# Optimization experiments

Measured on AMD Instinct MI355X. Metric: run time of the kernel, lower is better.

The kernel has to match this reference:

```python
import jax, jax.numpy as jnp
import numpy as np

N_ENTITIES = 100000
N_RELATIONS = 1000
D = 100   # embedding_size
K = 4     # tensor slices
B = 4096  # batch


def setup_inputs() -> dict:
    key = jax.random.key(0)
    k1, k2, k3, k4, k5, k6, k7, k8 = jax.random.split(key, 8)
    return {
        "heads": jax.random.randint(k1, (B,), 0, N_ENTITIES),
        "tails": jax.random.randint(k2, (B,), 0, N_ENTITIES),
        "relations": jax.random.randint(k3, (B,), 0, N_RELATIONS),
        # parameters, matching tf.random_uniform(0, 1)
        "entity_embedding": jax.random.uniform(k4, (N_ENTITIES, D), dtype=jnp.float32),
        "W": jax.random.uniform(k5, (N_RELATIONS, K, D, D), dtype=jnp.float32),
        "V": jax.random.uniform(k6, (N_RELATIONS, K, 2 * D), dtype=jnp.float32),
        "Bp": jax.random.uniform(k7, (N_RELATIONS, K), dtype=jnpp_f32 if False else jnp.float32),
        "U": jax.random.uniform(k8, (N_RELATIONS, K), dtype=jnp.float32),
    }


def reference(heads, tails, relations, entity_embedding, W, V, Bp, U):
    # gathers
    e1 = entity_embedding[heads]          # [B, D]
    e2 = entity_embedding[tails]          # [B, D]
    w = W[relations]                      # [B, K, D, D]
    v = V[relations]                      # [B, K, 2D]
    b = Bp[relations]                     # [B, K]
    u = U[relations]                      # [B, K]

    # g_a = v @ [e1; e2]
    e12 = jnp.concatenate([e1, e2], axis=1)           # [B, 2D]
    g_a = jnp.einsum('bkm,bm->bk', v, e12)            # [B, K]
    # g_b = e1^T W_k e2 (bilinear tensor product)
    g_b = jnp.einsum('bd,bkde,be->bk', e1, w, e2)     # [B, K]

    score = jnp.einsum('bk,bk->b', u, jnp.tanh(g_a + g_b + b))  # [B]
    pred = jax.nn.sigmoid(score)
    return pred
```

## Files before the change

kernel.cpp:

```cpp
#include <hip/hip_runtime.h>
#include <math.h>

#define D 100
#define K 4
#define NREL 1000
#define CH 8
#define NT 512

__global__ __launch_bounds__(1024) void k_group(
    const int* __restrict__ rels, const int* __restrict__ heads,
    const int* __restrict__ tails, int B,
    int* __restrict__ start, int* __restrict__ bb,
    int* __restrict__ bh, int* __restrict__ bt)
{
    __shared__ int sA[1024], sB[1024];
    const int tid = threadIdx.x;
    sA[tid] = 0;
    __syncthreads();
    for (int b = tid; b < B; b += 1024) atomicAdd(&sA[rels[b]], 1);
    __syncthreads();
    const int v = sA[tid];
    int* src = sA; int* dst = sB;
    for (int off = 1; off < 1024; off <<= 1) {
        int x = src[tid];
        if (tid >= off) x += src[tid - off];
        dst[tid] = x;
        __syncthreads();
        int* t = src; src = dst; dst = t;
    }
    const int excl = src[tid] - v;
    if (tid < NREL) start[tid] = excl;
    if (tid == 0)   start[NREL] = B;
    int* cur = dst;
    cur[tid] = excl;
    __syncthreads();
    for (int b = tid; b < B; b += 1024) {
        const int r = rels[b];
        const int pos = atomicAdd(&cur[r], 1);
        bb[pos] = b;
        bh[pos] = heads[b];
        bt[pos] = tails[b];
    }
}

#define WLOAD(u) const float4 wv##u = Wg4[(bat10 + (u)*2 + dsub) * 25 + c];
#define WFMA(u) { \
    const int drow = gbase + bat10 + (u)*2 + dsub; \
    _Pragma("unroll") \
    for (int it = 0; it < CH; ++it) { \
        acc[it] += (wv##u.x * e2r[it].x + wv##u.y * e2r[it].y \
                  + wv##u.z * e2r[it].z + wv##u.w * e2r[it].w) * e12[it][drow]; \
    } }

__global__ __launch_bounds__(NT, 4) void ntn_main(
    const float* __restrict__ E, const float* __restrict__ W,
    const float* __restrict__ V, const float* __restrict__ Bp,
    const float* __restrict__ U, const int* __restrict__ start,
    const int* __restrict__ bb, const int* __restrict__ bh,
    const int* __restrict__ bt, float* __restrict__ out)
{
    const int r  = blockIdx.x;
    const int cs = start[r];
    const int n  = start[r + 1] - cs;
    if (n <= 0) return;

    const int tid  = threadIdx.x;
    const int lane = tid & 63;
    const int w    = tid >> 6;
    const int k    = w & 3;
    const int g    = w >> 2;
    const int dsub = lane / 25;
    const int c    = lane % 25;
    const bool active = (lane < 50);
    const int gbase = g * 50;

    __shared__ float e12[CH][2 * D];
    __shared__ float red[8][CH];
    __shared__ int   ob[CH];

    const float4* Wg4 = reinterpret_cast<const float4*>(
        W + ((size_t)r * K + k) * D * D + (size_t)gbase * D);
    const float*  Vk  = V + ((size_t)r * K + k) * 2 * D;
    const float4* E4  = reinterpret_cast<const float4*>(E);

    for (int base = 0; base < n; base += CH) {
        const int m = min(CH, n - base);
        __syncthreads();
        if (tid < m) ob[tid] = bb[cs + base + tid];
        if (active && w < m) {
            const int idx = cs + base + w;
            const int ent = dsub ? bt[idx] : bh[idx];
            *(float4*)&e12[w][dsub * D + c * 4] = E4[(size_t)ent * 25 + c];
        }
        __syncthreads();

        float4 e2r[CH];
        #pragma unroll
        for (int it = 0; it < CH; ++it)
            e2r[it] = *(const float4*)&e12[it][D + c * 4];

        float acc[CH];
        #pragma unroll
        for (int it = 0; it < CH; ++it) acc[it] = 0.f;

        if (active) {
            #pragma unroll 1
            for (int bat = 0; bat < 5; ++bat) {
                const int bat10 = bat * 10;
                WLOAD(0) WLOAD(1) WLOAD(2) WLOAD(3) WLOAD(4)
                WFMA(0) WFMA(1) WFMA(2) WFMA(3) WFMA(4)
            }
        }
        if (g == 0) {
            for (int j = lane; j < 2 * D; j += 64) {
                const float vv = Vk[j];
                #pragma unroll
                for (int it = 0; it < CH; ++it) acc[it] += vv * e12[it][j];
            }
        }
        #pragma unroll
        for (int it = 0; it < CH; ++it) {
            float s = acc[it];
            #pragma unroll
            for (int off = 32; off > 0; off >>= 1) s += __shfl_down(s, off, 64);
            if (lane == 0) red[w][it] = s;
        }
        __syncthreads();
        if (tid < m) {
            const int rb = r * K;
            float score = 0.f;
            #pragma unroll
            for (int kk = 0; kk < K; ++kk) {
                const float gv = red[kk][tid] + red[kk + 4][tid] + Bp[rb + kk];
                score += U[rb + kk] * tanhf(gv);
            }
            out[ob[tid]] = 1.f / (1.f + expf(-score));
        }
    }
}

extern "C" void kernel_launch(void* const* d_in, const int* in_sizes, int n_in,
                              void* d_out, int out_size, void* d_ws, size_t ws_size,
                              hipStream_t stream) {
    const int*   heads = (const int*)d_in[0];
    const int*   tails = (const int*)d_in[1];
    const int*   rels  = (const int*)d_in[2];
    const float* E     = (const float*)d_in[3];
    const float* W     = (const float*)d_in[4];
    const float* V     = (const float*)d_in[5];
    const float* Bp    = (const float*)d_in[6];
    const float* U     = (const float*)d_in[7];
    float* out = (float*)d_out;

    const int B = in_sizes[0];
    int* start = (int*)d_ws;
    int* bb    = start + 1024;
    int* bh    = bb + B;
    int* bt    = bh + B;

    k_group<<<1, 1024, 0, stream>>>(rels, heads, tails, B, start, bb, bh, bt);
    ntn_main<<<NREL, NT, 0, stream>>>(E, W, V, Bp, U, start, bb, bh, bt, out);
}
```

Measured before the change: 68.75 us.

## Split batch items across wave groups instead of splitting W rows

Reassigns work so each pair of wave groups handles four batch items over all 100 W rows, rather than both groups handling eight items over half the rows. This cuts accumulator registers, and the launch bound is raised to allow more blocks per CU. The trade-off is that each wave reads twice as many W rows, and one group sits idle when a relation has four or fewer items.

After: 69.70 us. About the same (+1.4%).

```diff
diff --git a/kernel.cpp b/kernel.cpp
--- a/kernel.cpp
+++ b/kernel.cpp
@@ -43,16 +43,13 @@
     }
 }
 
-#define WLOAD(u) const float4 wv##u = Wg4[(bat10 + (u)*2 + dsub) * 25 + c];
-#define WFMA(u) { \
-    const int drow = gbase + bat10 + (u)*2 + dsub; \
-    _Pragma("unroll") \
-    for (int it = 0; it < CH; ++it) { \
-        acc[it] += (wv##u.x * e2r[it].x + wv##u.y * e2r[it].y \
-                  + wv##u.z * e2r[it].z + wv##u.w * e2r[it].w) * e12[it][drow]; \
-    } }
+#define WFMA(u) { const int rr = r0 + 2*(u); \
+    acc0 += (wv##u.x*e20.x + wv##u.y*e20.y + wv##u.z*e20.z + wv##u.w*e20.w) * e1p[0*2*D + rr]; \
+    acc1 += (wv##u.x*e21.x + wv##u.y*e21.y + wv##u.z*e21.z + wv##u.w*e21.w) * e1p[1*2*D + rr]; \
+    acc2 += (wv##u.x*e22.x + wv##u.y*e22.y + wv##u.z*e22.z + wv##u.w*e22.w) * e1p[2*2*D + rr]; \
+    acc3 += (wv##u.x*e23.x + wv##u.y*e23.y + wv##u.z*e23.z + wv##u.w*e23.w) * e1p[3*2*D + rr]; }
 
-__global__ __launch_bounds__(NT, 4) void ntn_main(
+__global__ __launch_bounds__(NT, 8) void ntn_main(
     const float* __restrict__ E, const float* __restrict__ W,
     const float* __restrict__ V, const float* __restrict__ Bp,
     const float* __restrict__ U, const int* __restrict__ start,
@@ -68,18 +65,16 @@
     const int lane = tid & 63;
     const int w    = tid >> 6;
     const int k    = w & 3;
-    const int g    = w >> 2;
+    const int h    = w >> 2;
     const int dsub = lane / 25;
     const int c    = lane % 25;
     const bool active = (lane < 50);
-    const int gbase = g * 50;
 
     __shared__ float e12[CH][2 * D];
-    __shared__ float red[8][CH];
+    __shared__ float red[8][4];
     __shared__ int   ob[CH];
 
-    const float4* Wg4 = reinterpret_cast<const float4*>(
-        W + ((size_t)r * K + k) * D * D + (size_t)gbase * D);
+    const float4* Wk4 = reinterpret_cast<const float4*>(W + ((size_t)r * K + k) * D * D);
     const float*  Vk  = V + ((size_t)r * K + k) * 2 * D;
     const float4* E4  = reinterpret_cast<const float4*>(E);
 
@@ -94,44 +89,53 @@
         }
         __syncthreads();
 
-        float4 e2r[CH];
-        #pragma unroll
-        for (int it = 0; it < CH; ++it)
-            e2r[it] = *(const float4*)&e12[it][D + c * 4];
+        float acc0 = 0.f, acc1 = 0.f, acc2 = 0.f, acc3 = 0.f;
+        if (h * 4 < m) {
+            const float* e1p = &e12[h * 4][0];
+            const float4 e20 = *(const float4*)&e12[h * 4 + 0][D + c * 4];
+            const float4 e21 = *(const float4*)&e12[h * 4 + 1][D + c * 4];
+            const float4 e22 = *(const float4*)&e12[h * 4 + 2][D + c * 4];
+            const float4 e23 = *(const float4*)&e12[h * 4 + 3][D + c * 4];
 
-        float acc[CH];
-        #pragma unroll
-        for (int it = 0; it < CH; ++it) acc[it] = 0.f;
-
-        if (active) {
-            #pragma unroll 1
-            for (int bat = 0; bat < 5; ++bat) {
-                const int bat10 = bat * 10;
-                WLOAD(0) WLOAD(1) WLOAD(2) WLOAD(3) WLOAD(4)
-                WFMA(0) WFMA(1) WFMA(2) WFMA(3) WFMA(4)
+            if (active) {
+                #pragma unroll 1
+                for (int bat = 0; bat < 10; ++bat) {
+                    const int r0 = bat * 10 + dsub;
+                    const float4 wv0 = Wk4[(r0    ) * 25 + c];
+                    const float4 wv1 = Wk4[(r0 + 2) * 25 + c];
+                    const float4 wv2 = Wk4[(r0 + 4) * 25 + c];
+                    const float4 wv3 = Wk4[(r0 + 6) * 25 + c];
+                    const float4 wv4 = Wk4[(r0 + 8) * 25 + c];
+                    WFMA(0) WFMA(1) WFMA(2) WFMA(3) WFMA(4)
+                }
             }
-        }
-        if (g == 0) {
             for (int j = lane; j < 2 * D; j += 64) {
                 const float vv = Vk[j];
-                #pragma unroll
-                for (int it = 0; it < CH; ++it) acc[it] += vv * e12[it][j];
+                acc0 += vv * e1p[0 * 2 * D + j];
+                acc1 += vv * e1p[1 * 2 * D + j];
+                acc2 += vv * e1p[2 * 2 * D + j];
+                acc3 += vv * e1p[3 * 2 * D + j];
             }
         }
         #pragma unroll
-        for (int it = 0; it < CH; ++it) {
-            float s = acc[it];
-            #pragma unroll
-            for (int off = 32; off > 0; off >>= 1) s += __shfl_down(s, off, 64);
-            if (lane == 0) red[w][it] = s;
+        for (int off = 32; off > 0; off >>= 1) {
+            acc0 += __shfl_down(acc0, off, 64);
+            acc1 += __shfl_down(acc1, off, 64);
+            acc2 += __shfl_down(acc2, off, 64);
+            acc3 += __shfl_down(acc3, off, 64);
+        }
+        if (lane == 0) {
+            red[w][0] = acc0; red[w][1] = acc1;
+            red[w][2] = acc2; red[w][3] = acc3;
         }
         __syncthreads();
         if (tid < m) {
             const int rb = r * K;
+            const int hr = (tid >> 2) * 4, il = tid & 3;
             float score = 0.f;
             #pragma unroll
             for (int kk = 0; kk < K; ++kk) {
-                const float gv = red[kk][tid] + red[kk + 4][tid] + Bp[rb + kk];
+                const float gv = red[hr + kk][il] + Bp[rb + kk];
                 score += U[rb + kk] * tanhf(gv);
             }
             out[ob[tid]] = 1.f / (1.f + expf(-score));
```
